# Performance work log

Hardware: AMD Instinct MI355X
Metric: run time of the kernel (lower is better)

Reference implementation:

```python
import jax, jax.numpy as jnp
import numpy as np

NUM_HEADS = 16
HEAD_DIM = 64  # hidden_size / num_heads


def setup_inputs() -> dict:
    key = jax.random.key(0)
    ks = jax.random.split(key, 20)
    B, S, H, K = 16, 1024, 1024, 64
    d = {"hidden_states": jax.random.normal(ks[0], (B, S, H), jnp.float32)}
    i = 1
    for p in ("q", "k", "v", "o"):
        d["W" + p] = jax.random.normal(ks[i], (H, H), jnp.float32) * (1.0 / np.sqrt(H)); i += 1
        d["b" + p] = jax.random.normal(ks[i], (H,), jnp.float32) * 0.02; i += 1
        d["LM" + p] = jax.random.normal(ks[i], (H, K), jnp.float32) * (1.0 / np.sqrt(K)); i += 1
        d["RM" + p] = jax.random.normal(ks[i], (K, H), jnp.float32) * (1.0 / np.sqrt(H)); i += 1
        d["F" + p] = jnp.ones((H,), jnp.float32)
    d["task"] = 0
    return d


def _proj(x, W, b, LM, RM, F):
    # RG weight reconstruction: weight = LM @ RM + W  (task==0 branch)
    w = LM @ RM + W  # [h_out, h_in]
    y = jnp.einsum("bsi,oi->bso", x, w) + b
    return y * F  # SFG per-channel scaling


def reference(hidden_states, Wq, bq, LMq, RMq, Fq, Wk, bk, LMk, RMk, Fk,
              Wv, bv, LMv, RMv, Fv, Wo, bo, LMo, RMo, Fo, task):
    B, S, H = hidden_states.shape
    nh, hd = NUM_HEADS, HEAD_DIM
    q = _proj(hidden_states, Wq, bq, LMq, RMq, Fq).reshape(B, S, nh, hd)
    k = _proj(hidden_states, Wk, bk, LMk, RMk, Fk).reshape(B, S, nh, hd)
    v = _proj(hidden_states, Wv, bv, LMv, RMv, Fv).reshape(B, S, nh, hd)
    scores = jnp.einsum("bqhd,bkhd->bhqk", q, k) / np.sqrt(hd).astype(np.float32)
    probs = jax.nn.softmax(scores, axis=-1)  # attn_dropout rate = 0.0
    ctx = jnp.einsum("bhqk,bkhd->bqhd", probs, v).reshape(B, S, H)
    out = _proj(ctx, Wo, bo, LMo, RMo, Fo)  # proj_dropout rate = 0.0
    return out
```

## Files before the change

### kernel.cpp

```cpp
#include <hip/hip_runtime.h>
#include <cstdint>
#include <cstddef>

typedef short short8 __attribute__((ext_vector_type(8)));
typedef float f32x4 __attribute__((ext_vector_type(4)));
typedef unsigned short us4 __attribute__((ext_vector_type(4)));

__device__ __forceinline__ unsigned short f2bf(float f) {
  unsigned int u = __float_as_uint(f);
  unsigned int r = (u + 0x7fffu + ((u >> 16) & 1u)) >> 16;
  return (unsigned short)r;
}
__device__ __forceinline__ float exp2_fast(float x) {
  return __builtin_amdgcn_exp2f(x);
}
__device__ __forceinline__ unsigned int cvt_pk_bf16(float a, float b) {
  unsigned int d;
  asm("v_cvt_pk_bf16_f32 %0, %1, %2" : "=v"(d) : "v"(a), "v"(b));
  return d;
}
__device__ __forceinline__ void gload_lds16(const void* g, void* l) {
  auto gp = reinterpret_cast<const __attribute__((address_space(1))) char*>(
      reinterpret_cast<uintptr_t>(g));
  auto lp = reinterpret_cast<__attribute__((address_space(3))) char*>(
      reinterpret_cast<uintptr_t>(l));
  __builtin_amdgcn_global_load_lds(gp, lp, 16, 0, 0);
}

__global__ __launch_bounds__(256) void prep_weights(
    const float* __restrict__ W, const float* __restrict__ bias,
    const float* __restrict__ LM, const float* __restrict__ RM,
    const float* __restrict__ F, float scale,
    unsigned short* __restrict__ Wout, float* __restrict__ bout) {
  const int o = blockIdx.x;
  const int tid = threadIdx.x;
  __shared__ float lm[64];
  if (tid < 64) lm[tid] = LM[o * 64 + tid];
  __syncthreads();
  const float f = F[o] * scale;
#pragma unroll
  for (int j = 0; j < 4; ++j) {
    const int i = tid + j * 256;
    float acc = W[o * 1024 + i];
#pragma unroll 16
    for (int k = 0; k < 64; ++k) acc = fmaf(lm[k], RM[k * 1024 + i], acc);
    Wout[o * 1024 + i] = f2bf(acc * f);
  }
  if (tid == 0) bout[o] = bias[o] * f;
}

__global__ __launch_bounds__(256) void cast_x(const float* __restrict__ x,
                                              unsigned short* __restrict__ y, int n4) {
  const int i = blockIdx.x * 256 + threadIdx.x;
  if (i >= n4) return;
  f32x4 v = *(const f32x4*)(x + (size_t)i * 4);
  us4 o;
  o[0] = f2bf(v[0]); o[1] = f2bf(v[1]); o[2] = f2bf(v[2]); o[3] = f2bf(v[3]);
  *(us4*)(y + (size_t)i * 4) = o;
}

template <int MODE>
__global__ __launch_bounds__(256) void gemm_bt(const unsigned short* __restrict__ A,
                                               const unsigned short* __restrict__ Bw,
                                               const float* __restrict__ bias,
                                               void* __restrict__ Cout,
                                               int M, int N, int K) {
  __shared__ unsigned short sA[128 * 64];
  __shared__ unsigned short sB[128 * 64];
  const int tid = threadIdx.x;
  const int w = tid >> 6;
  const int lane = tid & 63;
  const int quad = lane >> 4;
  const int ln = lane & 15;
  const int bm = blockIdx.x, bn = blockIdx.y;
  const int wm = w >> 1, wn = w & 1;

  f32x4 acc[4][4];
#pragma unroll
  for (int a = 0; a < 4; ++a)
#pragma unroll
    for (int b = 0; b < 4; ++b) acc[a][b] = (f32x4){0.f, 0.f, 0.f, 0.f};

  const size_t Kb = (size_t)K * 2;
  const char* Agb = (const char*)A + (size_t)bm * 128 * Kb;
  const char* Bgb = (const char*)Bw + (size_t)bn * 128 * Kb;
  char* sAb = (char*)sA;
  char* sBb = (char*)sB;
  const int sw = ln & 7;

  for (int k0 = 0; k0 < K; k0 += 64) {
    __syncthreads();
#pragma unroll
    for (int i = 0; i < 4; ++i) {
      const int Lb = w * 4096 + i * 1024 + lane * 16;
      const int r = Lb >> 7;
      const int c = (Lb >> 4) & 7;
      const int cb = ((c ^ (r & 7)) * 16);
      gload_lds16(Agb + (size_t)r * Kb + (size_t)k0 * 2 + cb, sAb + Lb);
      gload_lds16(Bgb + (size_t)r * Kb + (size_t)k0 * 2 + cb, sBb + Lb);
    }
    __syncthreads();
#pragma unroll
    for (int kk = 0; kk < 2; ++kk) {
      short8 af[4], bfv[4];
#pragma unroll
      for (int t = 0; t < 4; ++t) {
        const int ch = ((kk * 4 + quad) ^ sw) * 16;
        af[t]  = *(const short8*)(sAb + (wm * 64 + t * 16 + ln) * 128 + ch);
        bfv[t] = *(const short8*)(sBb + (wn * 64 + t * 16 + ln) * 128 + ch);
      }
#pragma unroll
      for (int mt = 0; mt < 4; ++mt)
#pragma unroll
        for (int nt = 0; nt < 4; ++nt)
          acc[mt][nt] = __builtin_amdgcn_mfma_f32_16x16x32_bf16(af[mt], bfv[nt], acc[mt][nt], 0, 0, 0);
    }
  }

  if (MODE == 0) {
    unsigned short* out = (unsigned short*)Cout;
#pragma unroll
    for (int mt = 0; mt < 4; ++mt) {
#pragma unroll
      for (int nt = 0; nt < 4; ++nt) {
        const int gn = bn * 128 + wn * 64 + nt * 16 + ln;
        const float bv = bias[gn];
        const int pidx = gn >> 10, rem = gn & 1023;
        const int hh = rem >> 6, dd = rem & 63;
        const int gm0 = bm * 128 + wm * 64 + mt * 16 + quad * 4;
        const int bb = gm0 >> 10, ss0 = gm0 & 1023;
        if (pidx < 2) {
#pragma unroll
          for (int r = 0; r < 4; ++r) {
            const size_t off = ((((size_t)pidx * 16 + bb) * 16 + hh) * 1024 + (ss0 + r)) * 64 + dd;
            out[off] = f2bf(acc[mt][nt][r] + bv);
          }
        } else {
          us4 pk;
#pragma unroll
          for (int r = 0; r < 4; ++r) pk[r] = f2bf(acc[mt][nt][r] + bv);
          const size_t off = (size_t)2 * 16777216 +
                             (((size_t)(bb * 16 + hh) * 64 + dd) * 1024 + ss0);
          *(us4*)(out + off) = pk;
        }
      }
    }
  } else {
    float* out = (float*)Cout;
#pragma unroll
    for (int mt = 0; mt < 4; ++mt) {
#pragma unroll
      for (int nt = 0; nt < 4; ++nt) {
        const int gn = bn * 128 + wn * 64 + nt * 16 + ln;
        const float bv = bias[gn];
#pragma unroll
        for (int r = 0; r < 4; ++r) {
          const int gm = bm * 128 + wm * 64 + mt * 16 + quad * 4 + r;
          out[(size_t)gm * N + gn] = acc[mt][nt][r] + bv;
        }
      }
    }
  }
}

__global__ __launch_bounds__(256) void attn(const unsigned short* __restrict__ Qb,
                                            const unsigned short* __restrict__ Kb_,
                                            const unsigned short* __restrict__ VTb,
                                            unsigned short* __restrict__ ctx) {
  __shared__ unsigned short sK[64 * 64];
  __shared__ unsigned short sVT[64 * 64];
  __shared__ unsigned short sP[128 * 72];
  const int tid = threadIdx.x;
  const int w = tid >> 6, lane = tid & 63, quad = lane >> 4, ln = lane & 15;
  const int bid = blockIdx.x;
  const int xcd = bid & 7, qt = (bid >> 3) & 7, sbh = bid >> 6;
  const int bh = xcd * 32 + sbh;
  const int b = bh >> 4, h = bh & 15;

  char* sKb = (char*)sK;
  char* sVb = (char*)sVT;
  char* sPb = (char*)sP;
  const int sw = ln & 7;

  short8 bq[2][2];
#pragma unroll
  for (int s = 0; s < 2; ++s) {
    const unsigned short* Qg =
        Qb + ((size_t)bh * 1024 + (size_t)qt * 128 + w * 32 + s * 16 + ln) * 64;
    bq[s][0] = *(const short8*)(Qg + quad * 8);
    bq[s][1] = *(const short8*)(Qg + 32 + quad * 8);
  }

  f32x4 accO[2][4];
#pragma unroll
  for (int s = 0; s < 2; ++s)
#pragma unroll
    for (int nt = 0; nt < 4; ++nt) accO[s][nt] = (f32x4){0.f, 0.f, 0.f, 0.f};
  float mrun[2] = {-3e38f, -3e38f}, lrun[2] = {0.f, 0.f};

  for (int kt = 0; kt < 16; ++kt) {
    __syncthreads();
    const char* Kg = (const char*)(Kb_ + ((size_t)bh * 1024 + (size_t)kt * 64) * 64);
    const char* Vg = (const char*)(VTb + (size_t)bh * 65536 + (size_t)kt * 64);
#pragma unroll
    for (int i = 0; i < 2; ++i) {
      const int Lb = w * 2048 + i * 1024 + lane * 16;
      const int r = Lb >> 7;
      const int c = (Lb >> 4) & 7;
      const int cb = ((c ^ (r & 7)) * 16);
      gload_lds16(Kg + (size_t)r * 128 + cb, sKb + Lb);
      gload_lds16(Vg + (size_t)r * 2048 + cb, sVb + Lb);
    }
    __syncthreads();

    f32x4 accS[2][4];
#pragma unroll
    for (int s = 0; s < 2; ++s)
#pragma unroll
      for (int mt = 0; mt < 4; ++mt) accS[s][mt] = (f32x4){0.f, 0.f, 0.f, 0.f};
#pragma unroll
    for (int kk = 0; kk < 2; ++kk) {
      short8 ak[4];
#pragma unroll
      for (int mt = 0; mt < 4; ++mt)
        ak[mt] = *(const short8*)(sKb + (mt * 16 + ln) * 128 + ((kk * 4 + quad) ^ sw) * 16);
#pragma unroll
      for (int s = 0; s < 2; ++s)
#pragma unroll
        for (int mt = 0; mt < 4; ++mt)
          accS[s][mt] = __builtin_amdgcn_mfma_f32_16x16x32_bf16(ak[mt], bq[s][kk], accS[s][mt], 0, 0, 0);
    }

#pragma unroll
    for (int s = 0; s < 2; ++s) {
      float tmax = -3e38f;
#pragma unroll
      for (int mt = 0; mt < 4; ++mt)
#pragma unroll
        for (int r = 0; r < 4; ++r) tmax = fmaxf(tmax, accS[s][mt][r]);
      tmax = fmaxf(tmax, __shfl_xor(tmax, 16));
      tmax = fmaxf(tmax, __shfl_xor(tmax, 32));
      const float mnew = fmaxf(mrun[s], tmax);
      const float alpha = exp2_fast(mrun[s] - mnew);
      mrun[s] = mnew;
      float psum = 0.f;
#pragma unroll
      for (int mt = 0; mt < 4; ++mt) {
        float p0 = exp2_fast(accS[s][mt][0] - mnew);
        float p1 = exp2_fast(accS[s][mt][1] - mnew);
        float p2 = exp2_fast(accS[s][mt][2] - mnew);
        float p3 = exp2_fast(accS[s][mt][3] - mnew);
        psum += (p0 + p1) + (p2 + p3);
        union { unsigned int u[2]; us4 v; } pu;
        pu.u[0] = cvt_pk_bf16(p0, p1);
        pu.u[1] = cvt_pk_bf16(p2, p3);
        *(us4*)(sP + (w * 32 + s * 16 + ln) * 72 + mt * 16 + quad * 4) = pu.v;
      }
      psum += __shfl_xor(psum, 16);
      psum += __shfl_xor(psum, 32);
      lrun[s] = lrun[s] * alpha + psum;
#pragma unroll
      for (int r = 0; r < 4; ++r) {
        const float ar = __shfl(alpha, quad * 4 + r);
#pragma unroll
        for (int nt = 0; nt < 4; ++nt) accO[s][nt][r] *= ar;
      }
    }

    asm volatile("" ::: "memory");

#pragma unroll
    for (int kk = 0; kk < 2; ++kk) {
      short8 ap[2];
#pragma unroll
      for (int s = 0; s < 2; ++s)
        ap[s] = *(const short8*)(sPb + (w * 32 + s * 16 + ln) * 144 + kk * 64 + quad * 16);
#pragma unroll
      for (int nt = 0; nt < 4; ++nt) {
        const short8 bv = *(const short8*)(sVb + (nt * 16 + ln) * 128 + ((kk * 4 + quad) ^ sw) * 16);
#pragma unroll
        for (int s = 0; s < 2; ++s)
          accO[s][nt] = __builtin_amdgcn_mfma_f32_16x16x32_bf16(ap[s], bv, accO[s][nt], 0, 0, 0);
      }
    }
  }

#pragma unroll
  for (int s = 0; s < 2; ++s) {
    const float inv = 1.0f / lrun[s];
#pragma unroll
    for (int r = 0; r < 4; ++r) {
      const float ivr = __shfl(inv, quad * 4 + r);
      const int sg = qt * 128 + w * 32 + s * 16 + quad * 4 + r;
#pragma unroll
      for (int nt = 0; nt < 4; ++nt) {
        const int d = nt * 16 + ln;
        ctx[((size_t)(b * 1024 + sg)) * 1024 + h * 64 + d] = f2bf(accO[s][nt][r] * ivr);
      }
    }
  }
}

extern "C" void kernel_launch(void* const* d_in, const int* in_sizes, int n_in,
                              void* d_out, int out_size, void* d_ws, size_t ws_size,
                              hipStream_t stream) {
  const float* hs  = (const float*)d_in[0];
  const float* Wq  = (const float*)d_in[1];
  const float* bq  = (const float*)d_in[2];
  const float* LMq = (const float*)d_in[3];
  const float* RMq = (const float*)d_in[4];
  const float* Fq  = (const float*)d_in[5];
  const float* Wk  = (const float*)d_in[6];
  const float* bk  = (const float*)d_in[7];
  const float* LMk = (const float*)d_in[8];
  const float* RMk = (const float*)d_in[9];
  const float* Fk  = (const float*)d_in[10];
  const float* Wv  = (const float*)d_in[11];
  const float* bv  = (const float*)d_in[12];
  const float* LMv = (const float*)d_in[13];
  const float* RMv = (const float*)d_in[14];
  const float* Fv  = (const float*)d_in[15];
  const float* Wo  = (const float*)d_in[16];
  const float* bo  = (const float*)d_in[17];
  const float* LMo = (const float*)d_in[18];
  const float* RMo = (const float*)d_in[19];
  const float* Fo  = (const float*)d_in[20];

  char* p = (char*)d_ws;
  unsigned short* xbf  = (unsigned short*)p; p += (size_t)16384 * 1024 * 2;
  unsigned short* Wqkv = (unsigned short*)p; p += (size_t)3072 * 1024 * 2;
  unsigned short* Wob  = (unsigned short*)p; p += (size_t)1024 * 1024 * 2;
  float* bqkv = (float*)p; p += 3072 * 4;
  float* bob  = (float*)p; p += 1024 * 4;
  unsigned short* qkv = (unsigned short*)p; p += (size_t)3 * 16777216 * 2;
  unsigned short* ctx = (unsigned short*)p; p += (size_t)16777216 * 2;

  const float qscale = 0.125f * 1.4426950408889634f;

  cast_x<<<16384, 256, 0, stream>>>(hs, xbf, 16777216 / 4);
  prep_weights<<<1024, 256, 0, stream>>>(Wq, bq, LMq, RMq, Fq, qscale, Wqkv, bqkv);
  prep_weights<<<1024, 256, 0, stream>>>(Wk, bk, LMk, RMk, Fk, 1.0f, Wqkv + 1024 * 1024, bqkv + 1024);
  prep_weights<<<1024, 256, 0, stream>>>(Wv, bv, LMv, RMv, Fv, 1.0f, Wqkv + 2 * 1024 * 1024, bqkv + 2048);
  prep_weights<<<1024, 256, 0, stream>>>(Wo, bo, LMo, RMo, Fo, 1.0f, Wob, bob);

  gemm_bt<0><<<dim3(128, 24), 256, 0, stream>>>(xbf, Wqkv, bqkv, (void*)qkv, 16384, 3072, 1024);

  attn<<<2048, 256, 0, stream>>>(qkv, qkv + 16777216, qkv + 2 * 16777216, ctx);

  gemm_bt<1><<<dim3(128, 8), 256, 0, stream>>>(ctx, Wob, bob, d_out, 16384, 1024, 1024);
}
```

Before: 505.1 us.

## Double-buffer K/V tiles in attention and skip rescaling with lazy max updates

The attention kernel now prefetches the next K/V tile into a second LDS buffer while computing on the current one, replacing the two per-iteration syncthreads with a vmcnt wait plus barriers. The online softmax only rescales the accumulator when the new max exceeds the running max by more than a threshold, and the row-sum cross-lane reduction is moved to the end. MFMA blocks are wrapped in s_setprio. This doubles K/V LDS usage, which may reduce occupancy, and adds a redundant final prefetch.

```diff
diff --git a/kernel.cpp b/kernel.cpp
--- a/kernel.cpp
+++ b/kernel.cpp
@@ -167,8 +167,8 @@
                                             const unsigned short* __restrict__ Kb_,
                                             const unsigned short* __restrict__ VTb,
                                             unsigned short* __restrict__ ctx) {
-  __shared__ unsigned short sK[64 * 64];
-  __shared__ unsigned short sVT[64 * 64];
+  __shared__ unsigned short sK[2][64 * 64];
+  __shared__ unsigned short sVT[2][64 * 64];
   __shared__ unsigned short sP[128 * 72];
   const int tid = threadIdx.x;
   const int w = tid >> 6, lane = tid & 63, quad = lane >> 4, ln = lane & 15;
@@ -177,8 +177,6 @@
   const int bh = xcd * 32 + sbh;
   const int b = bh >> 4, h = bh & 15;
 
-  char* sKb = (char*)sK;
-  char* sVb = (char*)sVT;
   char* sPb = (char*)sP;
   const int sw = ln & 7;
 
@@ -198,20 +196,32 @@
     for (int nt = 0; nt < 4; ++nt) accO[s][nt] = (f32x4){0.f, 0.f, 0.f, 0.f};
   float mrun[2] = {-3e38f, -3e38f}, lrun[2] = {0.f, 0.f};
 
-  for (int kt = 0; kt < 16; ++kt) {
-    __syncthreads();
-    const char* Kg = (const char*)(Kb_ + ((size_t)bh * 1024 + (size_t)kt * 64) * 64);
-    const char* Vg = (const char*)(VTb + (size_t)bh * 65536 + (size_t)kt * 64);
+  const char* Kbase = (const char*)Kb_ + (size_t)bh * 131072;
+  const char* Vbase = (const char*)VTb + (size_t)bh * 131072;
+
+  auto stage = [&](int kt, int buf) {
 #pragma unroll
     for (int i = 0; i < 2; ++i) {
       const int Lb = w * 2048 + i * 1024 + lane * 16;
       const int r = Lb >> 7;
       const int c = (Lb >> 4) & 7;
       const int cb = ((c ^ (r & 7)) * 16);
-      gload_lds16(Kg + (size_t)r * 128 + cb, sKb + Lb);
-      gload_lds16(Vg + (size_t)r * 2048 + cb, sVb + Lb);
-    }
-    __syncthreads();
+      gload_lds16(Kbase + (size_t)kt * 8192 + (size_t)r * 128 + cb, (char*)sK[buf] + Lb);
+      gload_lds16(Vbase + (size_t)kt * 128 + (size_t)r * 2048 + cb, (char*)sVT[buf] + Lb);
+    }
+  };
+
+  stage(0, 0);
+
+  for (int kt = 0; kt < 16; ++kt) {
+    const int cur = kt & 1;
+    char* sKb = (char*)sK[cur];
+    char* sVb = (char*)sVT[cur];
+
+    stage((kt + 1) & 15, cur ^ 1);
+    asm volatile("s_waitcnt vmcnt(4)" ::: "memory");
+    __builtin_amdgcn_s_barrier();
+    asm volatile("" ::: "memory");
 
     f32x4 accS[2][4];
 #pragma unroll
@@ -224,11 +234,13 @@
 #pragma unroll
       for (int mt = 0; mt < 4; ++mt)
         ak[mt] = *(const short8*)(sKb + (mt * 16 + ln) * 128 + ((kk * 4 + quad) ^ sw) * 16);
+      __builtin_amdgcn_s_setprio(1);
 #pragma unroll
       for (int s = 0; s < 2; ++s)
 #pragma unroll
         for (int mt = 0; mt < 4; ++mt)
           accS[s][mt] = __builtin_amdgcn_mfma_f32_16x16x32_bf16(ak[mt], bq[s][kk], accS[s][mt], 0, 0, 0);
+      __builtin_amdgcn_s_setprio(0);
     }
 
 #pragma unroll
@@ -240,31 +252,33 @@
         for (int r = 0; r < 4; ++r) tmax = fmaxf(tmax, accS[s][mt][r]);
       tmax = fmaxf(tmax, __shfl_xor(tmax, 16));
       tmax = fmaxf(tmax, __shfl_xor(tmax, 32));
-      const float mnew = fmaxf(mrun[s], tmax);
-      const float alpha = exp2_fast(mrun[s] - mnew);
-      mrun[s] = mnew;
+      if (!__all(tmax <= mrun[s] + 8.0f)) {
+        const float mnew = fmaxf(mrun[s], tmax);
+        const float alpha = exp2_fast(mrun[s] - mnew);
+        mrun[s] = mnew;
+        lrun[s] *= alpha;
+#pragma unroll
+        for (int r = 0; r < 4; ++r) {
+          const float ar = __shfl(alpha, quad * 4 + r);
+#pragma unroll
+          for (int nt = 0; nt < 4; ++nt) accO[s][nt][r] *= ar;
+        }
+      }
+      const float m = mrun[s];
       float psum = 0.f;
 #pragma unroll
       for (int mt = 0; mt < 4; ++mt) {
-        float p0 = exp2_fast(accS[s][mt][0] - mnew);
-        float p1 = exp2_fast(accS[s][mt][1] - mnew);
-        float p2 = exp2_fast(accS[s][mt][2] - mnew);
-        float p3 = exp2_fast(accS[s][mt][3] - mnew);
+        float p0 = exp2_fast(accS[s][mt][0] - m);
+        float p1 = exp2_fast(accS[s][mt][1] - m);
+        float p2 = exp2_fast(accS[s][mt][2] - m);
+        float p3 = exp2_fast(accS[s][mt][3] - m);
         psum += (p0 + p1) + (p2 + p3);
         union { unsigned int u[2]; us4 v; } pu;
         pu.u[0] = cvt_pk_bf16(p0, p1);
         pu.u[1] = cvt_pk_bf16(p2, p3);
         *(us4*)(sP + (w * 32 + s * 16 + ln) * 72 + mt * 16 + quad * 4) = pu.v;
       }
-      psum += __shfl_xor(psum, 16);
-      psum += __shfl_xor(psum, 32);
-      lrun[s] = lrun[s] * alpha + psum;
-#pragma unroll
-      for (int r = 0; r < 4; ++r) {
-        const float ar = __shfl(alpha, quad * 4 + r);
-#pragma unroll
-        for (int nt = 0; nt < 4; ++nt) accO[s][nt][r] *= ar;
-      }
+      lrun[s] += psum;
     }
 
     asm volatile("" ::: "memory");
@@ -278,16 +292,24 @@
 #pragma unroll
       for (int nt = 0; nt < 4; ++nt) {
         const short8 bv = *(const short8*)(sVb + (nt * 16 + ln) * 128 + ((kk * 4 + quad) ^ sw) * 16);
+        __builtin_amdgcn_s_setprio(1);
 #pragma unroll
         for (int s = 0; s < 2; ++s)
           accO[s][nt] = __builtin_amdgcn_mfma_f32_16x16x32_bf16(ap[s], bv, accO[s][nt], 0, 0, 0);
-      }
-    }
+        __builtin_amdgcn_s_setprio(0);
+      }
+    }
+
+    __builtin_amdgcn_s_barrier();
+    asm volatile("" ::: "memory");
   }
 
 #pragma unroll
   for (int s = 0; s < 2; ++s) {
-    const float inv = 1.0f / lrun[s];
+    float l = lrun[s];
+    l += __shfl_xor(l, 16);
+    l += __shfl_xor(l, 32);
+    const float inv = 1.0f / l;
 #pragma unroll
     for (int r = 0; r < 4; ++r) {
       const float ivr = __shfl(inv, quad * 4 + r);
```

Result: faster. 485.9 us (-3.8%).
